# Kernel tuning notes

Hardware: AMD Instinct MI355X
Metric: run time of the kernel (lower is better)

Reference implementation:

```python
import jax, jax.numpy as jnp
import numpy as np

DICE_TH = 0.4
CLS_TH = 0.5
LN_EPS = 1e-5


def setup_inputs() -> dict:
    key = jax.random.key(0)
    P, C, NC, K = 200_000, 256, 200, 24  # points, clicks, classes, latent prototypes
    ks = jax.random.split(key, 6)
    # structured masks: each click targets one of K prototype regions so the
    # dice/cls thresholds yield a non-degenerate grouping
    point_proto = jax.random.randint(ks[0], (P,), 0, K)
    proto_vals = jax.random.uniform(ks[1], (P,))
    click_proto = jax.random.randint(ks[2], (C,), 0, K)
    base = (point_proto[:, None] == click_proto[None, :]).astype(jnp.float32)  # [P, C]
    noise = jax.random.uniform(ks[3], (P, C))
    masks_heatmap = base * (0.6 + 0.4 * proto_vals[:, None]) + 0.02 * noise
    class_emb = jax.random.normal(ks[4], (K, NC)) * 3.0
    cls_logits = class_emb[click_proto] + 0.3 * jax.random.normal(ks[5], (C, NC))
    clicks_list = jax.random.randint(ks[0], (C,), 0, NC)  # unused (random_clicks=True)
    return {"masks_heatmap": masks_heatmap, "cls_logits": cls_logits,
            "clicks_list": clicks_list}


def _associate(masks_heatmap, cls_logits):
    """Greedy dice+cls-similarity grouping (random_clicks=True path).
    Returns labels[c] = leader click index of the group containing click c."""
    M = masks_heatmap                      # [P, C]
    C = M.shape[1]
    s = M.sum(0)                           # [C]
    # dice[i, j] = 2 * m_i . m_j / (sum(m_i) + sum(m_j))  (all pairs at once)
    dice = 2.0 * (M.T @ M) / (s[:, None] + s[None, :])
    # F.layer_norm over last dim, no affine
    mu = cls_logits.mean(-1, keepdims=True)
    var = ((cls_logits - mu) ** 2).mean(-1, keepdims=True)
    p = (cls_logits - mu) / jnp.sqrt(var + LN_EPS)
    sim = p @ p.T                          # [C, C]
    cond = (dice > DICE_TH) & (sim > CLS_TH)

    def step(carry, x):
        assigned, labels = carry
        i, row = x
        # skip if i already suppressed; take unsuppressed clicks matching row i
        take = row & (~assigned) & (~assigned[i])
        return (assigned | take, jnp.where(take, i, labels)), None

    init = (jnp.zeros((C,), bool), jnp.full((C,), -1, jnp.int32))
    (assigned, labels), _ = jax.lax.scan(
        step, init, (jnp.arange(C, dtype=jnp.int32), cond))
    return labels


def _merge(labels, masks_heatmap, cls_logits):
    """reduction='max': per-group max over member clicks. Unused group slots
    (non-leader indices) are zero-filled and flagged by group_valid."""
    C = masks_heatmap.shape[1]
    seg = jnp.where(labels >= 0, labels, C)  # route unassigned to dump segment
    counts = jax.ops.segment_sum(jnp.ones((C,), jnp.float32), seg,
                                 num_segments=C + 1)[:C]
    group_valid = counts > 0
    nm = jax.ops.segment_max(masks_heatmap.T, seg, num_segments=C + 1)[:C]  # [C, P]
    nc = jax.ops.segment_max(cls_logits, seg, num_segments=C + 1)[:C]      # [C, NC]
    new_masks = jnp.where(group_valid[:, None], nm, 0.0).T  # [P, C]
    new_cls = jnp.where(group_valid[:, None], nc, 0.0)      # [C, NC]
    return new_masks, new_cls, group_valid


def reference(masks_heatmap, cls_logits, clicks_list):
    labels = _associate(masks_heatmap, cls_logits)
    new_masks, new_cls, group_valid = _merge(labels, masks_heatmap, cls_logits)
    return labels, group_valid, new_masks, new_cls
```

## Files before the change

### kernel.cpp

```cpp
#include <hip/hip_runtime.h>
#include <cstdint>
#include <cstddef>

constexpr int P  = 200000;
constexpr int C  = 256;
constexpr int NC = 200;
#define DICE_TH 0.4f
#define CLS_TH  0.5f
#define LN_EPS  1e-5f

constexpr int KC = 800;
constexpr int NCHUNK = 250;
constexpr int NSTEP = KC / 32;
constexpr int GP_CHUNK = 3 * 16384;

constexpr size_t WS_GP      = 0;
constexpr size_t WS_G       = 49152000;
constexpr size_t WS_S       = WS_G + 262144;
constexpr size_t WS_PROW    = WS_S + 1024;
constexpr size_t WS_PT      = WS_PROW + 204800;
constexpr size_t WS_COND    = WS_PT + 204800;
constexpr size_t WS_MSTART  = WS_COND + 8192;
constexpr size_t WS_MEMBERS = WS_MSTART + 1280;

typedef float floatx16 __attribute__((ext_vector_type(16)));
typedef __bf16 bf16x8 __attribute__((ext_vector_type(8)));
typedef unsigned short ushort8 __attribute__((ext_vector_type(8)));

__device__ __forceinline__ unsigned short f2bf(float f) {
  unsigned u = __builtin_bit_cast(unsigned, f);
  unsigned r = u + 0x7FFFu + ((u >> 16) & 1u);
  return (unsigned short)(r >> 16);
}

constexpr int LDA = 40;

__global__ __launch_bounds__(256, 3) void gram_mfma_kernel(
    const float* __restrict__ M, float* __restrict__ Gp,
    float* __restrict__ s) {
  __shared__ unsigned short Abf[128 * LDA];
  __shared__ unsigned short Bbf[128 * LDA];

  const int type = blockIdx.x;
  const int i0 = (type == 2) ? 128 : 0;
  const int j0 = (type == 0) ? 0 : 128;
  const bool diag = (type != 1);
  const int tid = threadIdx.x;
  const int wv = tid >> 6, lane = tid & 63;
  const int c = tid & 127, h = tid >> 7;
  const int k0 = blockIdx.y * KC;

  floatx16 acc[4];
#pragma unroll
  for (int t = 0; t < 4; ++t)
#pragma unroll
    for (int r = 0; r < 16; ++r) acc[t][r] = 0.f;
  float ssum = 0.f;

  const int mrow = lane & 31;
  const int kgrp = (lane >> 5) * 8;

  float va[16], vb[16];
  {
    const float* colA = M + (size_t)(k0 + h * 16) * 256 + i0 + c;
#pragma unroll
    for (int u = 0; u < 16; ++u) va[u] = colA[(size_t)u * 256];
    if (!diag) {
      const float* colB = M + (size_t)(k0 + h * 16) * 256 + j0 + c;
#pragma unroll
      for (int u = 0; u < 16; ++u) vb[u] = colB[(size_t)u * 256];
    }
  }

  for (int step = 0; step < NSTEP; ++step) {
    {
      if (diag) {
#pragma unroll
        for (int u = 0; u < 16; ++u) ssum += va[u];
      }
      ushort8 lo, hi;
#pragma unroll
      for (int u = 0; u < 8; ++u) { lo[u] = f2bf(va[u]); hi[u] = f2bf(va[u + 8]); }
      *reinterpret_cast<ushort8*>(&Abf[c * LDA + h * 16]) = lo;
      *reinterpret_cast<ushort8*>(&Abf[c * LDA + h * 16 + 8]) = hi;
      if (!diag) {
#pragma unroll
        for (int u = 0; u < 8; ++u) { lo[u] = f2bf(vb[u]); hi[u] = f2bf(vb[u + 8]); }
        *reinterpret_cast<ushort8*>(&Bbf[c * LDA + h * 16]) = lo;
        *reinterpret_cast<ushort8*>(&Bbf[c * LDA + h * 16 + 8]) = hi;
      }
    }
    __syncthreads();

    if (step + 1 < NSTEP) {
      const int kb = k0 + (step + 1) * 32 + h * 16;
      const float* colA = M + (size_t)kb * 256 + i0 + c;
#pragma unroll
      for (int u = 0; u < 16; ++u) va[u] = colA[(size_t)u * 256];
      if (!diag) {
        const float* colB = M + (size_t)kb * 256 + j0 + c;
#pragma unroll
        for (int u = 0; u < 16; ++u) vb[u] = colB[(size_t)u * 256];
      }
    }

    const unsigned short* Bsrc = diag ? Abf : Bbf;
#pragma unroll
    for (int sub = 0; sub < 2; ++sub) {
      const int ko = sub * 16 + kgrp;
      bf16x8 a = __builtin_bit_cast(
          bf16x8, *reinterpret_cast<const ushort8*>(
                      &Abf[(32 * wv + mrow) * LDA + ko]));
#pragma unroll
      for (int t = 0; t < 4; ++t) {
        bf16x8 b = __builtin_bit_cast(
            bf16x8, *reinterpret_cast<const ushort8*>(
                        &Bsrc[(32 * t + mrow) * LDA + ko]));
        acc[t] = __builtin_amdgcn_mfma_f32_32x32x16_bf16(a, b, acc[t], 0, 0, 0);
      }
    }
    __syncthreads();
  }

  float* base = Gp + (size_t)blockIdx.y * GP_CHUNK + type * 16384;
#pragma unroll
  for (int t = 0; t < 4; ++t) {
    float* dst = base + (((wv * 4 + t) * 64 + lane) * 16);
#pragma unroll
    for (int q = 0; q < 4; ++q) {
      float4 v = make_float4(acc[t][4 * q], acc[t][4 * q + 1],
                             acc[t][4 * q + 2], acc[t][4 * q + 3]);
      *reinterpret_cast<float4*>(dst + 4 * q) = v;
    }
  }
  if (diag) atomicAdd(&s[i0 + c], ssum);
}

__global__ __launch_bounds__(256) void reduce_g_kernel(
    const float* __restrict__ Gp, float* __restrict__ G) {
  const int e = blockIdx.x * 256 + threadIdx.x;
  const float* p = Gp + e;
  float s0 = 0.f, s1 = 0.f, s2 = 0.f, s3 = 0.f, s4 = 0.f;
  float s5 = 0.f, s6 = 0.f, s7 = 0.f, s8 = 0.f, s9 = 0.f;
  for (int ch = 0; ch < NCHUNK; ch += 10) {
    s0 += p[(size_t)(ch + 0) * GP_CHUNK];
    s1 += p[(size_t)(ch + 1) * GP_CHUNK];
    s2 += p[(size_t)(ch + 2) * GP_CHUNK];
    s3 += p[(size_t)(ch + 3) * GP_CHUNK];
    s4 += p[(size_t)(ch + 4) * GP_CHUNK];
    s5 += p[(size_t)(ch + 5) * GP_CHUNK];
    s6 += p[(size_t)(ch + 6) * GP_CHUNK];
    s7 += p[(size_t)(ch + 7) * GP_CHUNK];
    s8 += p[(size_t)(ch + 8) * GP_CHUNK];
    s9 += p[(size_t)(ch + 9) * GP_CHUNK];
  }
  const float sum = (((s0 + s1) + (s2 + s3)) + ((s4 + s5) + (s6 + s7))) +
                    (s8 + s9);

  const int tile = e >> 14;
  const int r = e & 15;
  const int lane = (e >> 4) & 63;
  const int wvt = (e >> 10) & 15;
  const int wv = wvt >> 2, tt = wvt & 3;
  const int i0 = (tile == 2) ? 128 : 0;
  const int j0 = (tile == 0) ? 0 : 128;
  const int gr = i0 + 32 * wv + (r & 3) + 8 * (r >> 2) + 4 * (lane >> 5);
  const int gc = j0 + 32 * tt + (lane & 31);
  G[(size_t)gr * 256 + gc] = sum;
  if (tile == 1) G[(size_t)gc * 256 + gr] = sum;
}

__global__ __launch_bounds__(64) void ln_kernel(const float* __restrict__ cls,
                                                float* __restrict__ p_row,
                                                float* __restrict__ pT) {
  const int c = blockIdx.x;
  const int t = threadIdx.x;
  const float* x = cls + (size_t)c * NC;
  float v0 = x[t];
  float v1 = x[t + 64];
  float v2 = (t < 72) ? x[t + 128] : 0.f;

  float sum = v0 + v1 + v2;
#pragma unroll
  for (int o = 32; o > 0; o >>= 1) sum += __shfl_xor(sum, o);
  const float mu = sum / (float)NC;

  float d0 = v0 - mu, d1 = v1 - mu, d2 = (t < 72) ? (v2 - mu) : 0.f;
  float sq = d0 * d0 + d1 * d1 + d2 * d2;
#pragma unroll
  for (int o = 32; o > 0; o >>= 1) sq += __shfl_xor(sq, o);
  const float var = sq / (float)NC;
  const float inv = 1.0f / sqrtf(var + LN_EPS);

  float p0 = d0 * inv, p1 = d1 * inv, p2 = d2 * inv;
  p_row[(size_t)c * NC + t] = p0;
  p_row[(size_t)c * NC + t + 64] = p1;
  pT[(size_t)t * C + c] = p0;
  pT[(size_t)(t + 64) * C + c] = p1;
  if (t < 72) {
    p_row[(size_t)c * NC + t + 128] = p2;
    pT[(size_t)(t + 128) * C + c] = p2;
  }
}

__global__ __launch_bounds__(256) void cond_kernel(
    const float* __restrict__ G, const float* __restrict__ s,
    const float* __restrict__ p_row, const float* __restrict__ pT,
    unsigned long long* __restrict__ condW) {
  __shared__ float pi[NC];
  const int i = blockIdx.x;
  const int j = threadIdx.x;
  if (j < NC) pi[j] = p_row[(size_t)i * NC + j];
  __syncthreads();

  const float si = s[i];
  const float sj = s[j];
  const float g = G[(size_t)i * C + j];
  const float dice = 2.f * g / (si + sj);

  float a0 = 0.f, a1 = 0.f, a2 = 0.f, a3 = 0.f;
#pragma unroll 2
  for (int k = 0; k < NC; k += 4) {
    a0 = fmaf(pi[k + 0], pT[(size_t)(k + 0) * C + j], a0);
    a1 = fmaf(pi[k + 1], pT[(size_t)(k + 1) * C + j], a1);
    a2 = fmaf(pi[k + 2], pT[(size_t)(k + 2) * C + j], a2);
    a3 = fmaf(pi[k + 3], pT[(size_t)(k + 3) * C + j], a3);
  }
  const float acc = (a0 + a1) + (a2 + a3);

  const bool cnd = (dice > DICE_TH) && (acc > CLS_TH);
  unsigned long long m = __ballot(cnd);
  if ((j & 63) == 0) condW[i * 4 + (j >> 6)] = m;
}

__global__ __launch_bounds__(64) void scan_kernel(
    const unsigned long long* __restrict__ condW,
    float* __restrict__ out_labels, float* __restrict__ out_valid,
    int* __restrict__ mstart, int* __restrict__ members) {
  __shared__ unsigned long long cS[C * 4];
  __shared__ int cnt[C];
  __shared__ int ms[C + 1];
  const int t = threadIdx.x;

  for (int idx = t; idx < C * 4; idx += 64) cS[idx] = condW[idx];
  for (int idx = t; idx < C; idx += 64) cnt[idx] = 0;
  __syncthreads();

  unsigned long long asg[4] = {0ull, 0ull, 0ull, 0ull};
  int lab[4] = {-1, -1, -1, -1};

  unsigned long long r0 = cS[0], r1 = cS[1], r2 = cS[2], r3 = cS[3];
  for (int i = 0; i < C; ++i) {
    const int nx = (i + 1 < C) ? (i + 1) * 4 : 0;
    unsigned long long n0 = cS[nx], n1 = cS[nx + 1], n2 = cS[nx + 2],
                       n3 = cS[nx + 3];
    const int w = i >> 6, b = i & 63;
    if (!((asg[w] >> b) & 1ull)) {
      unsigned long long tk;
      tk = r0 & ~asg[0]; asg[0] |= tk; if ((tk >> t) & 1ull) lab[0] = i;
      tk = r1 & ~asg[1]; asg[1] |= tk; if ((tk >> t) & 1ull) lab[1] = i;
      tk = r2 & ~asg[2]; asg[2] |= tk; if ((tk >> t) & 1ull) lab[2] = i;
      tk = r3 & ~asg[3]; asg[3] |= tk; if ((tk >> t) & 1ull) lab[3] = i;
    }
    r0 = n0; r1 = n1; r2 = n2; r3 = n3;
  }

#pragma unroll
  for (int w = 0; w < 4; ++w)
    if (lab[w] >= 0) atomicAdd(&cnt[lab[w]], 1);
  __syncthreads();

  if (t == 0) {
    ms[0] = 0;
    for (int c2 = 0; c2 < C; ++c2) ms[c2 + 1] = ms[c2] + cnt[c2];
  }
  __syncthreads();
  for (int idx = t; idx < C; idx += 64) cnt[idx] = ms[idx];
  __syncthreads();
#pragma unroll
  for (int w = 0; w < 4; ++w) {
    if (lab[w] >= 0) {
      int pos = atomicAdd(&cnt[lab[w]], 1);
      members[pos] = w * 64 + t;
    }
  }
#pragma unroll
  for (int w = 0; w < 4; ++w) {
    const int col = w * 64 + t;
    out_labels[col] = (float)lab[w];
    out_valid[col] = (ms[col + 1] > ms[col]) ? 1.0f : 0.0f;
  }
  for (int idx = t; idx < C + 1; idx += 64) mstart[idx] = ms[idx];
}

__global__ __launch_bounds__(256) void merge_masks_kernel(
    const float* __restrict__ M, const int* __restrict__ mstart,
    const int* __restrict__ members, float* __restrict__ out_masks) {
  __shared__ float rows[16 * 256];
  __shared__ int msS[C + 1];
  __shared__ int memS[C];
  const int tid = threadIdx.x;
  const size_t p0 = (size_t)blockIdx.x * 16;

  msS[tid] = mstart[tid];
  if (tid == 0) msS[C] = mstart[C];
  memS[tid] = members[tid];

  const float4* src = reinterpret_cast<const float4*>(M + p0 * 256);
#pragma unroll
  for (int it = 0; it < 4; ++it)
    reinterpret_cast<float4*>(rows)[it * 256 + tid] = src[it * 256 + tid];
  __syncthreads();

  const int st = msS[tid], en = msS[tid + 1];
  float mx[16];
  if (en > st) {
    const int m0 = memS[st];
#pragma unroll
    for (int r = 0; r < 16; ++r) mx[r] = rows[r * 256 + m0];
    for (int k = st + 1; k < en; ++k) {
      const int mm = memS[k];
#pragma unroll
      for (int r = 0; r < 16; ++r) mx[r] = fmaxf(mx[r], rows[r * 256 + mm]);
    }
  } else {
#pragma unroll
    for (int r = 0; r < 16; ++r) mx[r] = 0.f;
  }
#pragma unroll
  for (int r = 0; r < 16; ++r) out_masks[(p0 + r) * 256 + tid] = mx[r];
}

__global__ __launch_bounds__(256) void merge_cls_kernel(
    const float* __restrict__ cls, const int* __restrict__ mstart,
    const int* __restrict__ members, float* __restrict__ out_cls) {
  __shared__ int se[2];
  const int c = blockIdx.x;
  const int t = threadIdx.x;
  if (t < 2) se[t] = mstart[c + t];
  __syncthreads();
  const int st = se[0], en = se[1];
  if (t < NC) {
    float mx = 0.f;
    if (en > st) {
      mx = cls[(size_t)members[st] * NC + t];
      for (int k = st + 1; k < en; ++k)
        mx = fmaxf(mx, cls[(size_t)members[k] * NC + t]);
    }
    out_cls[(size_t)c * NC + t] = mx;
  }
}

extern "C" void kernel_launch(void* const* d_in, const int* in_sizes, int n_in,
                              void* d_out, int out_size, void* d_ws,
                              size_t ws_size, hipStream_t stream) {
  const float* M = (const float*)d_in[0];
  const float* cls = (const float*)d_in[1];

  float* out = (float*)d_out;
  char* ws = (char*)d_ws;
  float* Gp = (float*)(ws + WS_GP);
  float* G = (float*)(ws + WS_G);
  float* s = (float*)(ws + WS_S);
  float* p_row = (float*)(ws + WS_PROW);
  float* pT = (float*)(ws + WS_PT);
  unsigned long long* condW = (unsigned long long*)(ws + WS_COND);
  int* mstart = (int*)(ws + WS_MSTART);
  int* members = (int*)(ws + WS_MEMBERS);

  float* out_labels = out;
  float* out_valid = out + 256;
  float* out_masks = out + 512;
  float* out_cls = out + 512 + (size_t)P * 256;

  hipMemsetAsync(ws + WS_S, 0, 1024, stream);

  gram_mfma_kernel<<<dim3(3, NCHUNK), 256, 0, stream>>>(M, Gp, s);
  reduce_g_kernel<<<GP_CHUNK / 256, 256, 0, stream>>>(Gp, G);
  ln_kernel<<<C, 64, 0, stream>>>(cls, p_row, pT);
  cond_kernel<<<C, 256, 0, stream>>>(G, s, p_row, pT, condW);
  scan_kernel<<<1, 64, 0, stream>>>(condW, out_labels, out_valid, mstart,
                                    members);
  merge_masks_kernel<<<P / 16, 256, 0, stream>>>(M, mstart, members, out_masks);
  merge_cls_kernel<<<C, 256, 0, stream>>>(cls, mstart, members, out_cls);
}
```

Measured before the change: 472.4 us.

## Double-buffer Gram prefetch, widen partial-sum reduction, vectorize mask merge stores

The bf16 MFMA Gram kernel now keeps two register buffers and prefetches global data two K-steps ahead, so loads have more time to overlap the MFMA work. The partial-Gram reduction uses 25 independent accumulators instead of 10, giving more loads in flight per thread. The mask-merge kernel issues its global loads before staging the segment tables, and each thread now handles a 4x4 row/column tile with float4 stores. The risks are higher register pressure in the Gram kernel and more divergent inner loops in the merge kernel. Starting the max at zero instead of at the first member matches the reference only because the heatmaps are non-negative.

New measurement: 538.6 us. 14.0% more time.

```diff
diff --git a/kernel.cpp b/kernel.cpp
--- a/kernel.cpp
+++ b/kernel.cpp
@@ -60,67 +60,69 @@
   const int mrow = lane & 31;
   const int kgrp = (lane >> 5) * 8;
 
-  float va[16], vb[16];
-  {
-    const float* colA = M + (size_t)(k0 + h * 16) * 256 + i0 + c;
-#pragma unroll
-    for (int u = 0; u < 16; ++u) va[u] = colA[(size_t)u * 256];
-    if (!diag) {
-      const float* colB = M + (size_t)(k0 + h * 16) * 256 + j0 + c;
-#pragma unroll
-      for (int u = 0; u < 16; ++u) vb[u] = colB[(size_t)u * 256];
-    }
-  }
-
-  for (int step = 0; step < NSTEP; ++step) {
-    {
-      if (diag) {
-#pragma unroll
-        for (int u = 0; u < 16; ++u) ssum += va[u];
-      }
-      ushort8 lo, hi;
-#pragma unroll
-      for (int u = 0; u < 8; ++u) { lo[u] = f2bf(va[u]); hi[u] = f2bf(va[u + 8]); }
-      *reinterpret_cast<ushort8*>(&Abf[c * LDA + h * 16]) = lo;
-      *reinterpret_cast<ushort8*>(&Abf[c * LDA + h * 16 + 8]) = hi;
-      if (!diag) {
-#pragma unroll
-        for (int u = 0; u < 8; ++u) { lo[u] = f2bf(vb[u]); hi[u] = f2bf(vb[u + 8]); }
-        *reinterpret_cast<ushort8*>(&Bbf[c * LDA + h * 16]) = lo;
-        *reinterpret_cast<ushort8*>(&Bbf[c * LDA + h * 16 + 8]) = hi;
-      }
-    }
-    __syncthreads();
-
-    if (step + 1 < NSTEP) {
-      const int kb = k0 + (step + 1) * 32 + h * 16;
-      const float* colA = M + (size_t)kb * 256 + i0 + c;
-#pragma unroll
-      for (int u = 0; u < 16; ++u) va[u] = colA[(size_t)u * 256];
-      if (!diag) {
-        const float* colB = M + (size_t)kb * 256 + j0 + c;
-#pragma unroll
-        for (int u = 0; u < 16; ++u) vb[u] = colB[(size_t)u * 256];
-      }
-    }
-
-    const unsigned short* Bsrc = diag ? Abf : Bbf;
-#pragma unroll
-    for (int sub = 0; sub < 2; ++sub) {
-      const int ko = sub * 16 + kgrp;
-      bf16x8 a = __builtin_bit_cast(
-          bf16x8, *reinterpret_cast<const ushort8*>(
-                      &Abf[(32 * wv + mrow) * LDA + ko]));
-#pragma unroll
-      for (int t = 0; t < 4; ++t) {
-        bf16x8 b = __builtin_bit_cast(
-            bf16x8, *reinterpret_cast<const ushort8*>(
-                        &Bsrc[(32 * t + mrow) * LDA + ko]));
-        acc[t] = __builtin_amdgcn_mfma_f32_32x32x16_bf16(a, b, acc[t], 0, 0, 0);
-      }
-    }
-    __syncthreads();
-  }
+  const float* colA0 = M + i0 + c;
+  const float* colB0 = M + j0 + c;
+
+  float va0[16], vb0[16], va1[16], vb1[16];
+
+#define LOADSTEP(VA, VB, STEP)                                            \
+  {                                                                       \
+    const size_t kb = (size_t)(k0 + (STEP)*32 + h * 16) * 256;            \
+    _Pragma("unroll") for (int u = 0; u < 16; ++u)                        \
+        VA[u] = colA0[kb + (size_t)u * 256];                              \
+    if (!diag) {                                                          \
+      _Pragma("unroll") for (int u = 0; u < 16; ++u)                      \
+          VB[u] = colB0[kb + (size_t)u * 256];                            \
+    }                                                                     \
+  }
+
+#define BODYSTEP(VA, VB, PF)                                              \
+  {                                                                       \
+    if (diag) {                                                           \
+      _Pragma("unroll") for (int u = 0; u < 16; ++u) ssum += VA[u];       \
+    }                                                                     \
+    ushort8 lo, hi;                                                       \
+    _Pragma("unroll") for (int u = 0; u < 8; ++u) {                       \
+      lo[u] = f2bf(VA[u]); hi[u] = f2bf(VA[u + 8]);                       \
+    }                                                                     \
+    *reinterpret_cast<ushort8*>(&Abf[c * LDA + h * 16]) = lo;             \
+    *reinterpret_cast<ushort8*>(&Abf[c * LDA + h * 16 + 8]) = hi;         \
+    if (!diag) {                                                          \
+      _Pragma("unroll") for (int u = 0; u < 8; ++u) {                     \
+        lo[u] = f2bf(VB[u]); hi[u] = f2bf(VB[u + 8]);                     \
+      }                                                                   \
+      *reinterpret_cast<ushort8*>(&Bbf[c * LDA + h * 16]) = lo;           \
+      *reinterpret_cast<ushort8*>(&Bbf[c * LDA + h * 16 + 8]) = hi;       \
+    }                                                                     \
+    __syncthreads();                                                      \
+    if ((PF) < NSTEP) LOADSTEP(VA, VB, PF);                               \
+    const unsigned short* Bsrc = diag ? Abf : Bbf;                        \
+    _Pragma("unroll") for (int sub = 0; sub < 2; ++sub) {                 \
+      const int ko = sub * 16 + kgrp;                                     \
+      bf16x8 a = __builtin_bit_cast(                                      \
+          bf16x8, *reinterpret_cast<const ushort8*>(                      \
+                      &Abf[(32 * wv + mrow) * LDA + ko]));                \
+      _Pragma("unroll") for (int t = 0; t < 4; ++t) {                     \
+        bf16x8 b = __builtin_bit_cast(                                    \
+            bf16x8, *reinterpret_cast<const ushort8*>(                    \
+                        &Bsrc[(32 * t + mrow) * LDA + ko]));              \
+        acc[t] =                                                          \
+            __builtin_amdgcn_mfma_f32_32x32x16_bf16(a, b, acc[t], 0, 0, 0); \
+      }                                                                   \
+    }                                                                     \
+    __syncthreads();                                                      \
+  }
+
+  LOADSTEP(va0, vb0, 0);
+  LOADSTEP(va1, vb1, 1);
+  for (int sp = 0; sp < NSTEP - 1; sp += 2) {
+    BODYSTEP(va0, vb0, sp + 2);
+    BODYSTEP(va1, vb1, sp + 3);
+  }
+  BODYSTEP(va0, vb0, NSTEP);
+
+#undef LOADSTEP
+#undef BODYSTEP
 
   float* base = Gp + (size_t)blockIdx.y * GP_CHUNK + type * 16384;
 #pragma unroll
@@ -140,22 +142,16 @@
     const float* __restrict__ Gp, float* __restrict__ G) {
   const int e = blockIdx.x * 256 + threadIdx.x;
   const float* p = Gp + e;
-  float s0 = 0.f, s1 = 0.f, s2 = 0.f, s3 = 0.f, s4 = 0.f;
-  float s5 = 0.f, s6 = 0.f, s7 = 0.f, s8 = 0.f, s9 = 0.f;
-  for (int ch = 0; ch < NCHUNK; ch += 10) {
-    s0 += p[(size_t)(ch + 0) * GP_CHUNK];
-    s1 += p[(size_t)(ch + 1) * GP_CHUNK];
-    s2 += p[(size_t)(ch + 2) * GP_CHUNK];
-    s3 += p[(size_t)(ch + 3) * GP_CHUNK];
-    s4 += p[(size_t)(ch + 4) * GP_CHUNK];
-    s5 += p[(size_t)(ch + 5) * GP_CHUNK];
-    s6 += p[(size_t)(ch + 6) * GP_CHUNK];
-    s7 += p[(size_t)(ch + 7) * GP_CHUNK];
-    s8 += p[(size_t)(ch + 8) * GP_CHUNK];
-    s9 += p[(size_t)(ch + 9) * GP_CHUNK];
-  }
-  const float sum = (((s0 + s1) + (s2 + s3)) + ((s4 + s5) + (s6 + s7))) +
-                    (s8 + s9);
+  float a[25];
+#pragma unroll
+  for (int i = 0; i < 25; ++i) a[i] = 0.f;
+  for (int ch = 0; ch < NCHUNK; ch += 25) {
+#pragma unroll
+    for (int i = 0; i < 25; ++i) a[i] += p[(size_t)(ch + i) * GP_CHUNK];
+  }
+  float sum = 0.f;
+#pragma unroll
+  for (int i = 0; i < 25; ++i) sum += a[i];
 
   const int tile = e >> 14;
   const int r = e & 15;
@@ -302,33 +298,44 @@
   const int tid = threadIdx.x;
   const size_t p0 = (size_t)blockIdx.x * 16;
 
+  const float4* src = reinterpret_cast<const float4*>(M + p0 * 256);
+  float4 v0 = src[0 * 256 + tid];
+  float4 v1 = src[1 * 256 + tid];
+  float4 v2 = src[2 * 256 + tid];
+  float4 v3 = src[3 * 256 + tid];
   msS[tid] = mstart[tid];
   if (tid == 0) msS[C] = mstart[C];
   memS[tid] = members[tid];
-
-  const float4* src = reinterpret_cast<const float4*>(M + p0 * 256);
-#pragma unroll
-  for (int it = 0; it < 4; ++it)
-    reinterpret_cast<float4*>(rows)[it * 256 + tid] = src[it * 256 + tid];
-  __syncthreads();
-
-  const int st = msS[tid], en = msS[tid + 1];
-  float mx[16];
-  if (en > st) {
-    const int m0 = memS[st];
-#pragma unroll
-    for (int r = 0; r < 16; ++r) mx[r] = rows[r * 256 + m0];
-    for (int k = st + 1; k < en; ++k) {
+  reinterpret_cast<float4*>(rows)[0 * 256 + tid] = v0;
+  reinterpret_cast<float4*>(rows)[1 * 256 + tid] = v1;
+  reinterpret_cast<float4*>(rows)[2 * 256 + tid] = v2;
+  reinterpret_cast<float4*>(rows)[3 * 256 + tid] = v3;
+  __syncthreads();
+
+  const int cb = (tid & 63) * 4;
+  const int rb = (tid >> 6) * 4;
+  float mx[4][4];
+#pragma unroll
+  for (int r = 0; r < 4; ++r)
+#pragma unroll
+    for (int cc = 0; cc < 4; ++cc) mx[r][cc] = 0.f;
+
+#pragma unroll
+  for (int cc = 0; cc < 4; ++cc) {
+    const int col = cb + cc;
+    const int st = msS[col], en = msS[col + 1];
+    for (int k = st; k < en; ++k) {
       const int mm = memS[k];
 #pragma unroll
-      for (int r = 0; r < 16; ++r) mx[r] = fmaxf(mx[r], rows[r * 256 + mm]);
-    }
-  } else {
-#pragma unroll
-    for (int r = 0; r < 16; ++r) mx[r] = 0.f;
-  }
-#pragma unroll
-  for (int r = 0; r < 16; ++r) out_masks[(p0 + r) * 256 + tid] = mx[r];
+      for (int r = 0; r < 4; ++r)
+        mx[r][cc] = fmaxf(mx[r][cc], rows[(rb + r) * 256 + mm]);
+    }
+  }
+#pragma unroll
+  for (int r = 0; r < 4; ++r) {
+    float4 v = make_float4(mx[r][0], mx[r][1], mx[r][2], mx[r][3]);
+    *reinterpret_cast<float4*>(&out_masks[(p0 + rb + r) * 256 + cb]) = v;
+  }
 }
 
 __global__ __launch_bounds__(256) void merge_cls_kernel(
```

## Compute full symmetric Gram tile per block to read each K-chunk once

Applied to the files above, without the earlier changes.

The three-block-per-chunk Gram computation (two diagonal 128x128 tiles plus one off-diagonal tile) is replaced by one block per K chunk that loads all 256 columns once into LDS and computes all three sub-tiles with 12 MFMA accumulators per wave. This removes the redundant global reads of M, since the off-diagonal block previously re-read both halves, and the duplicated bf16 conversion. The cost is fewer blocks (250 instead of 750), more registers at occupancy 1, and less latency hiding. The reduction kernel is remapped to the new partial layout and unrolls 25 chunks at a time.

After: 455.4 us. -3.6%, faster.

```diff
diff --git a/kernel.cpp b/kernel.cpp
--- a/kernel.cpp
+++ b/kernel.cpp
@@ -12,7 +12,7 @@
 constexpr int KC = 800;
 constexpr int NCHUNK = 250;
 constexpr int NSTEP = KC / 32;
-constexpr int GP_CHUNK = 3 * 16384;
+constexpr int GP_CHUNK = 48 * 1024;
 
 constexpr size_t WS_GP      = 0;
 constexpr size_t WS_G       = 49152000;
@@ -35,97 +35,82 @@
 
 constexpr int LDA = 40;
 
-__global__ __launch_bounds__(256, 3) void gram_mfma_kernel(
+__global__ __launch_bounds__(256, 1) void gram_full_kernel(
     const float* __restrict__ M, float* __restrict__ Gp,
     float* __restrict__ s) {
-  __shared__ unsigned short Abf[128 * LDA];
-  __shared__ unsigned short Bbf[128 * LDA];
-
-  const int type = blockIdx.x;
-  const int i0 = (type == 2) ? 128 : 0;
-  const int j0 = (type == 0) ? 0 : 128;
-  const bool diag = (type != 1);
+  __shared__ unsigned short Bls[256 * LDA];
+
   const int tid = threadIdx.x;
   const int wv = tid >> 6, lane = tid & 63;
-  const int c = tid & 127, h = tid >> 7;
-  const int k0 = blockIdx.y * KC;
-
-  floatx16 acc[4];
-#pragma unroll
-  for (int t = 0; t < 4; ++t)
+  const int k0 = blockIdx.x * KC;
+  const int mrow = lane & 31;
+  const int kgrp = (lane >> 5) * 8;
+
+  floatx16 acc[12];
+#pragma unroll
+  for (int t = 0; t < 12; ++t)
 #pragma unroll
     for (int r = 0; r < 16; ++r) acc[t][r] = 0.f;
   float ssum = 0.f;
 
-  const int mrow = lane & 31;
-  const int kgrp = (lane >> 5) * 8;
-
-  float va[16], vb[16];
+  const float* col0 = M + tid;
+  float va[32];
   {
-    const float* colA = M + (size_t)(k0 + h * 16) * 256 + i0 + c;
-#pragma unroll
-    for (int u = 0; u < 16; ++u) va[u] = colA[(size_t)u * 256];
-    if (!diag) {
-      const float* colB = M + (size_t)(k0 + h * 16) * 256 + j0 + c;
-#pragma unroll
-      for (int u = 0; u < 16; ++u) vb[u] = colB[(size_t)u * 256];
-    }
-  }
+    const size_t kb = (size_t)k0 * 256;
+#pragma unroll
+    for (int u = 0; u < 32; ++u) va[u] = col0[kb + (size_t)u * 256];
+  }
+
+#define FRAG(ROW, KO)                                                \
+  __builtin_bit_cast(bf16x8, *reinterpret_cast<const ushort8*>(      \
+                                 &Bls[((ROW) + mrow) * LDA + (KO)]))
 
   for (int step = 0; step < NSTEP; ++step) {
-    {
-      if (diag) {
-#pragma unroll
-        for (int u = 0; u < 16; ++u) ssum += va[u];
-      }
-      ushort8 lo, hi;
-#pragma unroll
-      for (int u = 0; u < 8; ++u) { lo[u] = f2bf(va[u]); hi[u] = f2bf(va[u + 8]); }
-      *reinterpret_cast<ushort8*>(&Abf[c * LDA + h * 16]) = lo;
-      *reinterpret_cast<ushort8*>(&Abf[c * LDA + h * 16 + 8]) = hi;
-      if (!diag) {
-#pragma unroll
-        for (int u = 0; u < 8; ++u) { lo[u] = f2bf(vb[u]); hi[u] = f2bf(vb[u + 8]); }
-        *reinterpret_cast<ushort8*>(&Bbf[c * LDA + h * 16]) = lo;
-        *reinterpret_cast<ushort8*>(&Bbf[c * LDA + h * 16 + 8]) = hi;
-      }
+#pragma unroll
+    for (int u = 0; u < 32; ++u) ssum += va[u];
+#pragma unroll
+    for (int q = 0; q < 4; ++q) {
+      ushort8 t8;
+#pragma unroll
+      for (int m = 0; m < 8; ++m) t8[m] = f2bf(va[q * 8 + m]);
+      *reinterpret_cast<ushort8*>(&Bls[tid * LDA + q * 8]) = t8;
     }
     __syncthreads();
 
     if (step + 1 < NSTEP) {
-      const int kb = k0 + (step + 1) * 32 + h * 16;
-      const float* colA = M + (size_t)kb * 256 + i0 + c;
-#pragma unroll
-      for (int u = 0; u < 16; ++u) va[u] = colA[(size_t)u * 256];
-      if (!diag) {
-        const float* colB = M + (size_t)kb * 256 + j0 + c;
-#pragma unroll
-        for (int u = 0; u < 16; ++u) vb[u] = colB[(size_t)u * 256];
-      }
-    }
-
-    const unsigned short* Bsrc = diag ? Abf : Bbf;
+      const size_t kb = (size_t)(k0 + (step + 1) * 32) * 256;
+#pragma unroll
+      for (int u = 0; u < 32; ++u) va[u] = col0[kb + (size_t)u * 256];
+    }
+
 #pragma unroll
     for (int sub = 0; sub < 2; ++sub) {
       const int ko = sub * 16 + kgrp;
-      bf16x8 a = __builtin_bit_cast(
-          bf16x8, *reinterpret_cast<const ushort8*>(
-                      &Abf[(32 * wv + mrow) * LDA + ko]));
-#pragma unroll
-      for (int t = 0; t < 4; ++t) {
-        bf16x8 b = __builtin_bit_cast(
-            bf16x8, *reinterpret_cast<const ushort8*>(
-                        &Bsrc[(32 * t + mrow) * LDA + ko]));
-        acc[t] = __builtin_amdgcn_mfma_f32_32x32x16_bf16(a, b, acc[t], 0, 0, 0);
+      bf16x8 a0 = FRAG(32 * wv, ko);
+      bf16x8 a1 = FRAG(128 + 32 * wv, ko);
+#pragma unroll
+      for (int cb = 0; cb < 4; ++cb) {
+        bf16x8 blo = FRAG(32 * cb, ko);
+        acc[cb] = __builtin_amdgcn_mfma_f32_32x32x16_bf16(a0, blo, acc[cb],
+                                                          0, 0, 0);
       }
+#pragma unroll
+      for (int cb = 0; cb < 4; ++cb) {
+        bf16x8 bhi = FRAG(128 + 32 * cb, ko);
+        acc[4 + cb] = __builtin_amdgcn_mfma_f32_32x32x16_bf16(
+            a0, bhi, acc[4 + cb], 0, 0, 0);
+        acc[8 + cb] = __builtin_amdgcn_mfma_f32_32x32x16_bf16(
+            a1, bhi, acc[8 + cb], 0, 0, 0);
+      }
     }
     __syncthreads();
   }
-
-  float* base = Gp + (size_t)blockIdx.y * GP_CHUNK + type * 16384;
-#pragma unroll
-  for (int t = 0; t < 4; ++t) {
-    float* dst = base + (((wv * 4 + t) * 64 + lane) * 16);
+#undef FRAG
+
+  float* base = Gp + (size_t)blockIdx.x * GP_CHUNK;
+#pragma unroll
+  for (int t = 0; t < 12; ++t) {
+    float* dst = base + (size_t)(wv * 12 + t) * 1024 + lane * 16;
 #pragma unroll
     for (int q = 0; q < 4; ++q) {
       float4 v = make_float4(acc[t][4 * q], acc[t][4 * q + 1],
@@ -133,41 +118,43 @@
       *reinterpret_cast<float4*>(dst + 4 * q) = v;
     }
   }
-  if (diag) atomicAdd(&s[i0 + c], ssum);
+  atomicAdd(&s[tid], ssum);
 }
 
 __global__ __launch_bounds__(256) void reduce_g_kernel(
     const float* __restrict__ Gp, float* __restrict__ G) {
   const int e = blockIdx.x * 256 + threadIdx.x;
   const float* p = Gp + e;
-  float s0 = 0.f, s1 = 0.f, s2 = 0.f, s3 = 0.f, s4 = 0.f;
-  float s5 = 0.f, s6 = 0.f, s7 = 0.f, s8 = 0.f, s9 = 0.f;
-  for (int ch = 0; ch < NCHUNK; ch += 10) {
-    s0 += p[(size_t)(ch + 0) * GP_CHUNK];
-    s1 += p[(size_t)(ch + 1) * GP_CHUNK];
-    s2 += p[(size_t)(ch + 2) * GP_CHUNK];
-    s3 += p[(size_t)(ch + 3) * GP_CHUNK];
-    s4 += p[(size_t)(ch + 4) * GP_CHUNK];
-    s5 += p[(size_t)(ch + 5) * GP_CHUNK];
-    s6 += p[(size_t)(ch + 6) * GP_CHUNK];
-    s7 += p[(size_t)(ch + 7) * GP_CHUNK];
-    s8 += p[(size_t)(ch + 8) * GP_CHUNK];
-    s9 += p[(size_t)(ch + 9) * GP_CHUNK];
-  }
-  const float sum = (((s0 + s1) + (s2 + s3)) + ((s4 + s5) + (s6 + s7))) +
-                    (s8 + s9);
-
-  const int tile = e >> 14;
-  const int r = e & 15;
-  const int lane = (e >> 4) & 63;
-  const int wvt = (e >> 10) & 15;
-  const int wv = wvt >> 2, tt = wvt & 3;
-  const int i0 = (tile == 2) ? 128 : 0;
-  const int j0 = (tile == 0) ? 0 : 128;
-  const int gr = i0 + 32 * wv + (r & 3) + 8 * (r >> 2) + 4 * (lane >> 5);
-  const int gc = j0 + 32 * tt + (lane & 31);
+  float a[25];
+#pragma unroll
+  for (int i = 0; i < 25; ++i) a[i] = 0.f;
+  for (int ch = 0; ch < NCHUNK; ch += 25) {
+#pragma unroll
+    for (int i = 0; i < 25; ++i) a[i] += p[(size_t)(ch + i) * GP_CHUNK];
+  }
+  float sum = 0.f;
+#pragma unroll
+  for (int i = 0; i < 25; ++i) sum += a[i];
+
+  const int sub = e >> 10;
+  const int idx = e & 1023;
+  const int lane = idx >> 4;
+  const int r = idx & 15;
+  const int wv = sub / 12;
+  const int t = sub % 12;
+  int rowband, colband;
+  bool mirror = false;
+  if (t < 4) {
+    rowband = 32 * wv; colband = 32 * t;
+  } else if (t < 8) {
+    rowband = 32 * wv; colband = 128 + 32 * (t - 4); mirror = true;
+  } else {
+    rowband = 128 + 32 * wv; colband = 128 + 32 * (t - 8);
+  }
+  const int gr = rowband + (r & 3) + 8 * (r >> 2) + 4 * (lane >> 5);
+  const int gc = colband + (lane & 31);
   G[(size_t)gr * 256 + gc] = sum;
-  if (tile == 1) G[(size_t)gc * 256 + gr] = sum;
+  if (mirror) G[(size_t)gc * 256 + gr] = sum;
 }
 
 __global__ __launch_bounds__(64) void ln_kernel(const float* __restrict__ cls,
@@ -375,8 +362,8 @@
 
   hipMemsetAsync(ws + WS_S, 0, 1024, stream);
 
-  gram_mfma_kernel<<<dim3(3, NCHUNK), 256, 0, stream>>>(M, Gp, s);
-  reduce_g_kernel<<<GP_CHUNK / 256, 256, 0, stream>>>(Gp, G);
+  gram_full_kernel<<<NCHUNK, 256, 0, stream>>>(M, Gp, s);
+  reduce_g_kernel<<<GP_CHUNK / 1024 * 4, 256, 0, stream>>>(Gp, G);
   ln_kernel<<<C, 64, 0, stream>>>(cls, p_row, pT);
   cond_kernel<<<C, 256, 0, stream>>>(G, s, p_row, pT, condW);
   scan_kernel<<<1, 64, 0, stream>>>(condW, out_labels, out_valid, mstart,
```
